# Performance work log

Hardware: AMD Instinct MI355X
Metric: run time of the kernel (lower is better)

## Reference

```python
import jax, jax.numpy as jnp
import numpy as np

N_NODES = 50000
N_EDGES = 800000
IN_DIM = 64
OUT_DIM = 128
K = 2
FINAL_DIM = IN_DIM * (2 ** (K + 1))  # 512


def _mean_agg(h, src, dst, inv_deg, n):
    # mean over neighbors: message h[src] summed into dst, normalized by in-degree
    s = jax.ops.segment_sum(h[src], dst, num_segments=n)
    return s * inv_deg[:, None]


def setup_inputs() -> dict:
    key = jax.random.key(0)
    k1, k2, k3 = jax.random.split(key, 3)
    feature = jax.random.normal(k1, (N_NODES, IN_DIM), dtype=jnp.float32)
    edge_index = jax.random.randint(k2, (2, N_EDGES), 0, N_NODES, dtype=jnp.int64)
    W = jax.random.normal(k3, (OUT_DIM, FINAL_DIM), dtype=jnp.float32) * 0.02
    b = jnp.zeros((OUT_DIM,), dtype=jnp.float32)
    return {"feature": feature, "edge_index": edge_index, "W": W, "b": b}


def reference(feature, edge_index, W, b):
    n = feature.shape[0]
    src, dst = edge_index[0], edge_index[1]
    ones = jnp.ones((src.shape[0],), dtype=feature.dtype)
    # degree normalizers (clamped to 1) for mean aggregation, each direction
    deg_in = jax.ops.segment_sum(ones, dst, num_segments=n)
    deg_out = jax.ops.segment_sum(ones, src, num_segments=n)
    inv_in = 1.0 / jnp.maximum(deg_in, 1.0)
    inv_out = 1.0 / jnp.maximum(deg_out, 1.0)

    h = feature
    for _ in range(K + 1):  # K+1 directed hops; dim doubles each hop
        h_in = _mean_agg(h, src, dst, inv_in, n)   # aggregate from in-neighbors
        h_out = _mean_agg(h, dst, src, inv_out, n)  # aggregate from out-neighbors
        h = jnp.concatenate([h_in, h_out], axis=-1)

    # output linear projection: [N, FINAL_DIM] @ [FINAL_DIM, OUT_DIM]
    return h @ W.T + b
```

## Files before the change

### kernel.cpp

```cpp
#include <hip/hip_runtime.h>

#define NN 50000
#define NE 800000
#define NBUCK 100
#define BUCK_N 500
#define CAP 10016
#define PA_BLOCKS 500
#define PA_CHUNK 1600

typedef __attribute__((ext_vector_type(8))) short short8;
typedef __attribute__((ext_vector_type(4))) float floatx4;

__device__ __forceinline__ unsigned short f2b(float x) {
    unsigned u = __float_as_uint(x);
    return (unsigned short)((u + 0x7fffu + ((u >> 16) & 1u)) >> 16);
}
__device__ __forceinline__ unsigned pk2(float lo, float hi) {
    return (unsigned)f2b(lo) | ((unsigned)f2b(hi) << 16);
}
__device__ __forceinline__ float blo(unsigned u) { return __uint_as_float(u << 16); }
__device__ __forceinline__ float bhi(unsigned u) { return __uint_as_float(u & 0xffff0000u); }
__device__ __forceinline__ void acc8(uint4 u, float* a) {
    a[0] += blo(u.x); a[1] += bhi(u.x);
    a[2] += blo(u.y); a[3] += bhi(u.y);
    a[4] += blo(u.z); a[5] += bhi(u.z);
    a[6] += blo(u.w); a[7] += bhi(u.w);
}

__global__ void featb_kernel(const float4* __restrict__ f32, uint2* __restrict__ fb) {
    int idx = blockIdx.x * 256 + threadIdx.x;
    float4 v = f32[idx];
    fb[idx] = make_uint2(pk2(v.x, v.y), pk2(v.z, v.w));
}

__global__ __launch_bounds__(256) void bucket_kernel(const int* __restrict__ src,
                                                     const int* __restrict__ dst,
                                                     int* __restrict__ gcnt_in,
                                                     int* __restrict__ gcnt_out,
                                                     int2* __restrict__ pin,
                                                     int2* __restrict__ pout) {
    __shared__ int cin[NBUCK], cout[NBUCK], rin[NBUCK], rout[NBUCK];
    int tid = threadIdx.x;
    if (tid < NBUCK) { cin[tid] = 0; cout[tid] = 0; }
    __syncthreads();
    int e0 = blockIdx.x * PA_CHUNK, e1 = e0 + PA_CHUNK;
    for (int e = e0 + tid; e < e1; e += 256) {
        atomicAdd(&cin[dst[e] / BUCK_N], 1);
        atomicAdd(&cout[src[e] / BUCK_N], 1);
    }
    __syncthreads();
    if (tid < NBUCK) {
        rin[tid]  = atomicAdd(&gcnt_in[tid], cin[tid]);
        rout[tid] = atomicAdd(&gcnt_out[tid], cout[tid]);
        cin[tid] = 0; cout[tid] = 0;
    }
    __syncthreads();
    for (int e = e0 + tid; e < e1; e += 256) {
        int s = src[e], d = dst[e];
        int bi = d / BUCK_N;
        int p = atomicAdd(&cin[bi], 1);
        pin[(size_t)bi * CAP + rin[bi] + p] = make_int2(d, s);
        int bo = s / BUCK_N;
        int q = atomicAdd(&cout[bo], 1);
        pout[(size_t)bo * CAP + rout[bo] + q] = make_int2(s, d);
    }
}

__global__ void bucket_scan_kernel(const int* __restrict__ gcnt_in,
                                   const int* __restrict__ gcnt_out,
                                   int* __restrict__ bb_in, int* __restrict__ bb_out) {
    if (threadIdx.x == 0) {
        int run = 0;
        for (int b = 0; b < NBUCK; ++b) { bb_in[b] = run; run += gcnt_in[b]; }
    }
    if (threadIdx.x == 1) {
        int run = 0;
        for (int b = 0; b < NBUCK; ++b) { bb_out[b] = run; run += gcnt_out[b]; }
    }
}

__global__ __launch_bounds__(1024) void csr_build_kernel(const int2* __restrict__ pin,
                                                         const int2* __restrict__ pout,
                                                         const int* __restrict__ gcnt_in,
                                                         const int* __restrict__ gcnt_out,
                                                         const int* __restrict__ bb_in,
                                                         const int* __restrict__ bb_out,
                                                         int* __restrict__ row_in,
                                                         int* __restrict__ row_out,
                                                         int* __restrict__ csr_in,
                                                         int* __restrict__ csr_out) {
    bool dirout = blockIdx.x >= NBUCK;
    int b = dirout ? blockIdx.x - NBUCK : blockIdx.x;
    const int2* pairs = (dirout ? pout : pin) + (size_t)b * CAP;
    int cnt  = dirout ? gcnt_out[b] : gcnt_in[b];
    int base = dirout ? bb_out[b] : bb_in[b];
    int* row = dirout ? row_out : row_in;
    int* csr = dirout ? csr_out : csr_in;
    int lo = b * BUCK_N;
    __shared__ int deg[BUCK_N], incl[BUCK_N], cur[BUCK_N];
    int tid = threadIdx.x;
    if (tid < BUCK_N) { deg[tid] = 0; cur[tid] = 0; }
    __syncthreads();
    for (int i = tid; i < cnt; i += 1024) atomicAdd(&deg[pairs[i].x - lo], 1);
    __syncthreads();
    if (tid < BUCK_N) incl[tid] = deg[tid];
    __syncthreads();
    for (int off = 1; off < BUCK_N; off <<= 1) {
        int v = 0;
        if (tid < BUCK_N && tid >= off) v = incl[tid - off];
        __syncthreads();
        if (tid < BUCK_N) incl[tid] += v;
        __syncthreads();
    }
    if (tid < BUCK_N) row[lo + tid] = base + incl[tid] - deg[tid];
    if (tid == 0 && b == NBUCK - 1) row[NN] = base + incl[BUCK_N - 1];
    __syncthreads();
    for (int i = tid; i < cnt; i += 1024) {
        int2 pr = pairs[i];
        int li = pr.x - lo;
        int pos = atomicAdd(&cur[li], 1);
        csr[base + incl[li] - deg[li] + pos] = pr.y;
    }
}

__global__ void gather1_kernel(const uint4* __restrict__ feat,
                               const int* __restrict__ row_in, const int* __restrict__ csr_in,
                               const int* __restrict__ row_out, const int* __restrict__ csr_out,
                               uint4* __restrict__ h1) {
    unsigned idx = blockIdx.x * 256 + threadIdx.x;
    unsigned n = idx >> 4, r = idx & 15;
    bool is_out = (r >= 8);
    unsigned f = r & 7;
    const int* row = is_out ? row_out : row_in;
    const int* csr = is_out ? csr_out : csr_in;
    int beg = row[n], end = row[n + 1];
    float inv = 1.0f / fmaxf((float)(end - beg), 1.0f);
    float a[8] = {};
    int j = beg;
    for (; j + 7 < end; j += 8) {
        uint4 u0 = feat[(size_t)csr[j] * 8 + f];
        uint4 u1 = feat[(size_t)csr[j + 1] * 8 + f];
        uint4 u2 = feat[(size_t)csr[j + 2] * 8 + f];
        uint4 u3 = feat[(size_t)csr[j + 3] * 8 + f];
        uint4 u4 = feat[(size_t)csr[j + 4] * 8 + f];
        uint4 u5 = feat[(size_t)csr[j + 5] * 8 + f];
        uint4 u6 = feat[(size_t)csr[j + 6] * 8 + f];
        uint4 u7 = feat[(size_t)csr[j + 7] * 8 + f];
        acc8(u0, a); acc8(u1, a); acc8(u2, a); acc8(u3, a);
        acc8(u4, a); acc8(u5, a); acc8(u6, a); acc8(u7, a);
    }
    for (; j < end; ++j) acc8(feat[(size_t)csr[j] * 8 + f], a);
    uint4 o;
    o.x = pk2(a[0] * inv, a[1] * inv);
    o.y = pk2(a[2] * inv, a[3] * inv);
    o.z = pk2(a[4] * inv, a[5] * inv);
    o.w = pk2(a[6] * inv, a[7] * inv);
    h1[(size_t)n * 16 + r] = o;
}

__global__ void gather2_kernel(const uint4* __restrict__ h1,
                               const int* __restrict__ row_in, const int* __restrict__ csr_in,
                               const int* __restrict__ row_out, const int* __restrict__ csr_out,
                               uint4* __restrict__ h2) {
    unsigned idx = blockIdx.x * 256 + threadIdx.x;
    unsigned n = idx >> 5, r = idx & 31;
    bool is_out = (r >= 16);
    unsigned f = r & 15;
    const int* row = is_out ? row_out : row_in;
    const int* csr = is_out ? csr_out : csr_in;
    int beg = row[n], end = row[n + 1];
    float inv = 1.0f / fmaxf((float)(end - beg), 1.0f);
    float a[8] = {};
    int j = beg;
    for (; j + 7 < end; j += 8) {
        uint4 u0 = h1[(size_t)csr[j] * 16 + f];
        uint4 u1 = h1[(size_t)csr[j + 1] * 16 + f];
        uint4 u2 = h1[(size_t)csr[j + 2] * 16 + f];
        uint4 u3 = h1[(size_t)csr[j + 3] * 16 + f];
        uint4 u4 = h1[(size_t)csr[j + 4] * 16 + f];
        uint4 u5 = h1[(size_t)csr[j + 5] * 16 + f];
        uint4 u6 = h1[(size_t)csr[j + 6] * 16 + f];
        uint4 u7 = h1[(size_t)csr[j + 7] * 16 + f];
        acc8(u0, a); acc8(u1, a); acc8(u2, a); acc8(u3, a);
        acc8(u4, a); acc8(u5, a); acc8(u6, a); acc8(u7, a);
    }
    for (; j < end; ++j) acc8(h1[(size_t)csr[j] * 16 + f], a);
    uint4 o;
    o.x = pk2(a[0] * inv, a[1] * inv);
    o.y = pk2(a[2] * inv, a[3] * inv);
    o.z = pk2(a[4] * inv, a[5] * inv);
    o.w = pk2(a[6] * inv, a[7] * inv);
    h2[(size_t)n * 32 + r] = o;
}

__global__ void prep_b_kernel(const float* __restrict__ W, unsigned short* __restrict__ Bnk) {
    int idx = blockIdx.x * 256 + threadIdx.x;
    int n = idx >> 8, k = idx & 255;
    float v = (n < 128) ? W[n * 512 + k] : W[(n - 128) * 512 + 256 + k];
    Bnk[idx] = f2b(v);
}

__global__ __launch_bounds__(256) void gemm_mfma_kernel(const unsigned short* __restrict__ A,
                                                        const unsigned short* __restrict__ Bnk,
                                                        unsigned short* __restrict__ C) {
    __shared__ unsigned short Bs[16][264];
    __shared__ unsigned short Cb[4][16][264];
    int tid = threadIdx.x;
    int wave = tid >> 6, lane = tid & 63;
    int l15 = lane & 15, q = lane >> 4;
    int m0 = blockIdx.x * 64;
    int mrow = m0 + wave * 16 + l15;
    int mclamp = min(mrow, NN - 1);
    const unsigned short* Arow = A + (size_t)mclamp * 256;
    short8 af[8];
#pragma unroll
    for (int s = 0; s < 8; ++s)
        af[s] = *(const short8*)(Arow + s * 32 + q * 8);
    floatx4 acc[16];
#pragma unroll
    for (int c = 0; c < 16; ++c) acc[c] = (floatx4){0.f, 0.f, 0.f, 0.f};
#pragma unroll
    for (int c = 0; c < 16; ++c) {
        {
            int nl = tid >> 4, seg = tid & 15;
            const uint4* srcp = (const uint4*)(Bnk + ((size_t)(16 * c + nl)) * 256 + seg * 16);
            uint4 v0 = srcp[0], v1 = srcp[1];
            *(uint4*)&Bs[nl][seg * 16] = v0;
            *(uint4*)&Bs[nl][seg * 16 + 8] = v1;
        }
        __syncthreads();
#pragma unroll
        for (int s = 0; s < 8; ++s) {
            short8 bf = *(const short8*)&Bs[l15][s * 32 + q * 8];
            acc[c] = __builtin_amdgcn_mfma_f32_16x16x32_bf16(af[s], bf, acc[c], 0, 0, 0);
        }
        __syncthreads();
    }
#pragma unroll
    for (int c = 0; c < 16; ++c)
#pragma unroll
        for (int r = 0; r < 4; ++r)
            Cb[wave][q * 4 + r][16 * c + l15] = f2b(acc[c][r]);
    __syncthreads();
#pragma unroll
    for (int i = 0; i < 8; ++i) {
        int t = i * 64 + lane;
        int rrow = t >> 5;
        int seg = t & 31;
        int m = m0 + wave * 16 + rrow;
        if (m < NN) {
            uint4 v = *(const uint4*)&Cb[wave][rrow][seg * 8];
            *(uint4*)(C + (size_t)m * 256 + seg * 8) = v;
        }
    }
}

__global__ void final_kernel(const uint4* __restrict__ g,
                             const int* __restrict__ row_in, const int* __restrict__ csr_in,
                             const int* __restrict__ row_out, const int* __restrict__ csr_out,
                             const float4* __restrict__ b4, float4* __restrict__ out) {
    unsigned idx = blockIdx.x * 256 + threadIdx.x;
    unsigned n = idx >> 4, f = idx & 15;
    float a[8] = {};
    {
        int beg = row_in[n], end = row_in[n + 1];
        float inv = 1.0f / fmaxf((float)(end - beg), 1.0f);
        float s[8] = {};
        int j = beg;
        for (; j + 7 < end; j += 8) {
            uint4 u0 = g[(size_t)csr_in[j] * 32 + f];
            uint4 u1 = g[(size_t)csr_in[j + 1] * 32 + f];
            uint4 u2 = g[(size_t)csr_in[j + 2] * 32 + f];
            uint4 u3 = g[(size_t)csr_in[j + 3] * 32 + f];
            uint4 u4 = g[(size_t)csr_in[j + 4] * 32 + f];
            uint4 u5 = g[(size_t)csr_in[j + 5] * 32 + f];
            uint4 u6 = g[(size_t)csr_in[j + 6] * 32 + f];
            uint4 u7 = g[(size_t)csr_in[j + 7] * 32 + f];
            acc8(u0, s); acc8(u1, s); acc8(u2, s); acc8(u3, s);
            acc8(u4, s); acc8(u5, s); acc8(u6, s); acc8(u7, s);
        }
        for (; j < end; ++j) acc8(g[(size_t)csr_in[j] * 32 + f], s);
#pragma unroll
        for (int i = 0; i < 8; ++i) a[i] += s[i] * inv;
    }
    {
        int beg = row_out[n], end = row_out[n + 1];
        float inv = 1.0f / fmaxf((float)(end - beg), 1.0f);
        float s[8] = {};
        int j = beg;
        for (; j + 7 < end; j += 8) {
            uint4 u0 = g[(size_t)csr_out[j] * 32 + 16 + f];
            uint4 u1 = g[(size_t)csr_out[j + 1] * 32 + 16 + f];
            uint4 u2 = g[(size_t)csr_out[j + 2] * 32 + 16 + f];
            uint4 u3 = g[(size_t)csr_out[j + 3] * 32 + 16 + f];
            uint4 u4 = g[(size_t)csr_out[j + 4] * 32 + 16 + f];
            uint4 u5 = g[(size_t)csr_out[j + 5] * 32 + 16 + f];
            uint4 u6 = g[(size_t)csr_out[j + 6] * 32 + 16 + f];
            uint4 u7 = g[(size_t)csr_out[j + 7] * 32 + 16 + f];
            acc8(u0, s); acc8(u1, s); acc8(u2, s); acc8(u3, s);
            acc8(u4, s); acc8(u5, s); acc8(u6, s); acc8(u7, s);
        }
        for (; j < end; ++j) acc8(g[(size_t)csr_out[j] * 32 + 16 + f], s);
#pragma unroll
        for (int i = 0; i < 8; ++i) a[i] += s[i] * inv;
    }
    float4 b0 = b4[2 * f], b1 = b4[2 * f + 1];
    out[(size_t)n * 32 + 2 * f]     = make_float4(a[0] + b0.x, a[1] + b0.y, a[2] + b0.z, a[3] + b0.w);
    out[(size_t)n * 32 + 2 * f + 1] = make_float4(a[4] + b1.x, a[5] + b1.y, a[6] + b1.z, a[7] + b1.w);
}

extern "C" void kernel_launch(void* const* d_in, const int* in_sizes, int n_in,
                              void* d_out, int out_size, void* d_ws, size_t ws_size,
                              hipStream_t stream) {
    const float* feature = (const float*)d_in[0];
    const int*   edges   = (const int*)d_in[1];
    const float* W       = (const float*)d_in[2];
    const float* b       = (const float*)d_in[3];
    const int* src = edges;
    const int* dst = edges + NE;
    float* out = (float*)d_out;

    unsigned short* featb = (unsigned short*)d_ws;
    unsigned short* h1b = featb + (size_t)NN * 64;
    unsigned short* h2b = h1b + (size_t)NN * 128;
    unsigned short* gb  = h2b + (size_t)NN * 256;
    unsigned short* Bnk = gb + (size_t)NN * 256;
    int2* pin  = (int2*)(Bnk + 65536);
    int2* pout = pin + (size_t)NBUCK * CAP;
    int* csr_in  = (int*)(pout + (size_t)NBUCK * CAP);
    int* csr_out = csr_in + NE;
    int* row_in  = csr_out + NE;
    int* row_out = row_in + NN + 1;
    int* gcnt_in  = row_out + NN + 1;
    int* gcnt_out = gcnt_in + 128;
    int* bb_in   = gcnt_out + 128;
    int* bb_out  = bb_in + 128;

    (void)hipMemsetAsync(gcnt_in, 0, 256 * sizeof(int), stream);
    featb_kernel<<<(NN * 16) / 256, 256, 0, stream>>>((const float4*)feature, (uint2*)featb);
    prep_b_kernel<<<256, 256, 0, stream>>>(W, Bnk);
    bucket_kernel<<<PA_BLOCKS, 256, 0, stream>>>(src, dst, gcnt_in, gcnt_out, pin, pout);
    bucket_scan_kernel<<<1, 64, 0, stream>>>(gcnt_in, gcnt_out, bb_in, bb_out);
    csr_build_kernel<<<2 * NBUCK, 1024, 0, stream>>>(pin, pout, gcnt_in, gcnt_out,
                                                     bb_in, bb_out, row_in, row_out,
                                                     csr_in, csr_out);

    gather1_kernel<<<(NN * 16) / 256, 256, 0, stream>>>(
        (const uint4*)featb, row_in, csr_in, row_out, csr_out, (uint4*)h1b);
    gather2_kernel<<<(NN * 32) / 256, 256, 0, stream>>>(
        (const uint4*)h1b, row_in, csr_in, row_out, csr_out, (uint4*)h2b);
    gemm_mfma_kernel<<<(NN + 63) / 64, 256, 0, stream>>>(h2b, Bnk, gb);
    final_kernel<<<(NN * 16) / 256, 256, 0, stream>>>(
        (const uint4*)gb, row_in, csr_in, row_out, csr_out, (const float4*)b, (float4*)out);
}
```

Measured before the change: 309.0 us.

## Merge prep kernels, halve gather unroll, double GEMM rows per block

Fuses the feature bf16 conversion and the weight-prep kernels into one launch that splits work by block index, removing one launch. Reduces the gather inner-loop unroll from 8 to 4 in the gather1, gather2 and final kernels, which lowers register pressure but leaves fewer loads in flight. The MFMA GEMM now handles 128 rows per block with two A tiles per wave, so each staged B tile is reused twice. That halves B reloads from global memory and barrier rounds per row, at the cost of more accumulator registers.

```diff
diff --git a/kernel.cpp b/kernel.cpp
--- a/kernel.cpp
+++ b/kernel.cpp
@@ -27,10 +27,19 @@
     a[6] += blo(u.w); a[7] += bhi(u.w);
 }
 
-__global__ void featb_kernel(const float4* __restrict__ f32, uint2* __restrict__ fb) {
-    int idx = blockIdx.x * 256 + threadIdx.x;
-    float4 v = f32[idx];
-    fb[idx] = make_uint2(pk2(v.x, v.y), pk2(v.z, v.w));
+__global__ void prep_kernel(const float4* __restrict__ f32, uint2* __restrict__ fb,
+                            const float* __restrict__ W, unsigned short* __restrict__ Bnk) {
+    int bid = blockIdx.x;
+    if (bid < 3125) {
+        int idx = bid * 256 + threadIdx.x;
+        float4 v = f32[idx];
+        fb[idx] = make_uint2(pk2(v.x, v.y), pk2(v.z, v.w));
+    } else {
+        int idx = (bid - 3125) * 256 + threadIdx.x;
+        int n = idx >> 8, k = idx & 255;
+        float v = (n < 128) ? W[n * 512 + k] : W[(n - 128) * 512 + 256 + k];
+        Bnk[idx] = f2b(v);
+    }
 }
 
 __global__ __launch_bounds__(256) void bucket_kernel(const int* __restrict__ src,
@@ -137,17 +146,12 @@
     float inv = 1.0f / fmaxf((float)(end - beg), 1.0f);
     float a[8] = {};
     int j = beg;
-    for (; j + 7 < end; j += 8) {
+    for (; j + 3 < end; j += 4) {
         uint4 u0 = feat[(size_t)csr[j] * 8 + f];
         uint4 u1 = feat[(size_t)csr[j + 1] * 8 + f];
         uint4 u2 = feat[(size_t)csr[j + 2] * 8 + f];
         uint4 u3 = feat[(size_t)csr[j + 3] * 8 + f];
-        uint4 u4 = feat[(size_t)csr[j + 4] * 8 + f];
-        uint4 u5 = feat[(size_t)csr[j + 5] * 8 + f];
-        uint4 u6 = feat[(size_t)csr[j + 6] * 8 + f];
-        uint4 u7 = feat[(size_t)csr[j + 7] * 8 + f];
         acc8(u0, a); acc8(u1, a); acc8(u2, a); acc8(u3, a);
-        acc8(u4, a); acc8(u5, a); acc8(u6, a); acc8(u7, a);
     }
     for (; j < end; ++j) acc8(feat[(size_t)csr[j] * 8 + f], a);
     uint4 o;
@@ -172,17 +176,12 @@
     float inv = 1.0f / fmaxf((float)(end - beg), 1.0f);
     float a[8] = {};
     int j = beg;
-    for (; j + 7 < end; j += 8) {
+    for (; j + 3 < end; j += 4) {
         uint4 u0 = h1[(size_t)csr[j] * 16 + f];
         uint4 u1 = h1[(size_t)csr[j + 1] * 16 + f];
         uint4 u2 = h1[(size_t)csr[j + 2] * 16 + f];
         uint4 u3 = h1[(size_t)csr[j + 3] * 16 + f];
-        uint4 u4 = h1[(size_t)csr[j + 4] * 16 + f];
-        uint4 u5 = h1[(size_t)csr[j + 5] * 16 + f];
-        uint4 u6 = h1[(size_t)csr[j + 6] * 16 + f];
-        uint4 u7 = h1[(size_t)csr[j + 7] * 16 + f];
         acc8(u0, a); acc8(u1, a); acc8(u2, a); acc8(u3, a);
-        acc8(u4, a); acc8(u5, a); acc8(u6, a); acc8(u7, a);
     }
     for (; j < end; ++j) acc8(h1[(size_t)csr[j] * 16 + f], a);
     uint4 o;
@@ -191,13 +190,6 @@
     o.z = pk2(a[4] * inv, a[5] * inv);
     o.w = pk2(a[6] * inv, a[7] * inv);
     h2[(size_t)n * 32 + r] = o;
-}
-
-__global__ void prep_b_kernel(const float* __restrict__ W, unsigned short* __restrict__ Bnk) {
-    int idx = blockIdx.x * 256 + threadIdx.x;
-    int n = idx >> 8, k = idx & 255;
-    float v = (n < 128) ? W[n * 512 + k] : W[(n - 128) * 512 + 256 + k];
-    Bnk[idx] = f2b(v);
 }
 
 __global__ __launch_bounds__(256) void gemm_mfma_kernel(const unsigned short* __restrict__ A,
@@ -208,17 +200,21 @@
     int tid = threadIdx.x;
     int wave = tid >> 6, lane = tid & 63;
     int l15 = lane & 15, q = lane >> 4;
-    int m0 = blockIdx.x * 64;
-    int mrow = m0 + wave * 16 + l15;
-    int mclamp = min(mrow, NN - 1);
-    const unsigned short* Arow = A + (size_t)mclamp * 256;
-    short8 af[8];
-#pragma unroll
-    for (int s = 0; s < 8; ++s)
-        af[s] = *(const short8*)(Arow + s * 32 + q * 8);
-    floatx4 acc[16];
-#pragma unroll
-    for (int c = 0; c < 16; ++c) acc[c] = (floatx4){0.f, 0.f, 0.f, 0.f};
+    int m0 = blockIdx.x * 128;
+    short8 af[2][8];
+#pragma unroll
+    for (int t = 0; t < 2; ++t) {
+        int mrow = m0 + (wave + 4 * t) * 16 + l15;
+        const unsigned short* Arow = A + (size_t)min(mrow, NN - 1) * 256;
+#pragma unroll
+        for (int s = 0; s < 8; ++s)
+            af[t][s] = *(const short8*)(Arow + s * 32 + q * 8);
+    }
+    floatx4 acc[2][16];
+#pragma unroll
+    for (int t = 0; t < 2; ++t)
+#pragma unroll
+        for (int c = 0; c < 16; ++c) acc[t][c] = (floatx4){0.f, 0.f, 0.f, 0.f};
 #pragma unroll
     for (int c = 0; c < 16; ++c) {
         {
@@ -232,26 +228,31 @@
 #pragma unroll
         for (int s = 0; s < 8; ++s) {
             short8 bf = *(const short8*)&Bs[l15][s * 32 + q * 8];
-            acc[c] = __builtin_amdgcn_mfma_f32_16x16x32_bf16(af[s], bf, acc[c], 0, 0, 0);
-        }
-        __syncthreads();
-    }
-#pragma unroll
-    for (int c = 0; c < 16; ++c)
-#pragma unroll
-        for (int r = 0; r < 4; ++r)
-            Cb[wave][q * 4 + r][16 * c + l15] = f2b(acc[c][r]);
-    __syncthreads();
-#pragma unroll
-    for (int i = 0; i < 8; ++i) {
-        int t = i * 64 + lane;
-        int rrow = t >> 5;
-        int seg = t & 31;
-        int m = m0 + wave * 16 + rrow;
-        if (m < NN) {
-            uint4 v = *(const uint4*)&Cb[wave][rrow][seg * 8];
-            *(uint4*)(C + (size_t)m * 256 + seg * 8) = v;
-        }
+            acc[0][c] = __builtin_amdgcn_mfma_f32_16x16x32_bf16(af[0][s], bf, acc[0][c], 0, 0, 0);
+            acc[1][c] = __builtin_amdgcn_mfma_f32_16x16x32_bf16(af[1][s], bf, acc[1][c], 0, 0, 0);
+        }
+        __syncthreads();
+    }
+#pragma unroll
+    for (int t = 0; t < 2; ++t) {
+#pragma unroll
+        for (int c = 0; c < 16; ++c)
+#pragma unroll
+            for (int r = 0; r < 4; ++r)
+                Cb[wave][q * 4 + r][16 * c + l15] = f2b(acc[t][c][r]);
+        __syncthreads();
+#pragma unroll
+        for (int i = 0; i < 8; ++i) {
+            int tt = i * 64 + lane;
+            int rrow = tt >> 5;
+            int seg = tt & 31;
+            int m = m0 + (wave + 4 * t) * 16 + rrow;
+            if (m < NN) {
+                uint4 v = *(const uint4*)&Cb[wave][rrow][seg * 8];
+                *(uint4*)(C + (size_t)m * 256 + seg * 8) = v;
+            }
+        }
+        __syncthreads();
     }
 }
 
@@ -267,17 +268,12 @@
         float inv = 1.0f / fmaxf((float)(end - beg), 1.0f);
         float s[8] = {};
         int j = beg;
-        for (; j + 7 < end; j += 8) {
+        for (; j + 3 < end; j += 4) {
             uint4 u0 = g[(size_t)csr_in[j] * 32 + f];
             uint4 u1 = g[(size_t)csr_in[j + 1] * 32 + f];
             uint4 u2 = g[(size_t)csr_in[j + 2] * 32 + f];
             uint4 u3 = g[(size_t)csr_in[j + 3] * 32 + f];
-            uint4 u4 = g[(size_t)csr_in[j + 4] * 32 + f];
-            uint4 u5 = g[(size_t)csr_in[j + 5] * 32 + f];
-            uint4 u6 = g[(size_t)csr_in[j + 6] * 32 + f];
-            uint4 u7 = g[(size_t)csr_in[j + 7] * 32 + f];
             acc8(u0, s); acc8(u1, s); acc8(u2, s); acc8(u3, s);
-            acc8(u4, s); acc8(u5, s); acc8(u6, s); acc8(u7, s);
         }
         for (; j < end; ++j) acc8(g[(size_t)csr_in[j] * 32 + f], s);
 #pragma unroll
@@ -288,17 +284,12 @@
         float inv = 1.0f / fmaxf((float)(end - beg), 1.0f);
         float s[8] = {};
         int j = beg;
-        for (; j + 7 < end; j += 8) {
+        for (; j + 3 < end; j += 4) {
             uint4 u0 = g[(size_t)csr_out[j] * 32 + 16 + f];
             uint4 u1 = g[(size_t)csr_out[j + 1] * 32 + 16 + f];
             uint4 u2 = g[(size_t)csr_out[j + 2] * 32 + 16 + f];
             uint4 u3 = g[(size_t)csr_out[j + 3] * 32 + 16 + f];
-            uint4 u4 = g[(size_t)csr_out[j + 4] * 32 + 16 + f];
-            uint4 u5 = g[(size_t)csr_out[j + 5] * 32 + 16 + f];
-            uint4 u6 = g[(size_t)csr_out[j + 6] * 32 + 16 + f];
-            uint4 u7 = g[(size_t)csr_out[j + 7] * 32 + 16 + f];
             acc8(u0, s); acc8(u1, s); acc8(u2, s); acc8(u3, s);
-            acc8(u4, s); acc8(u5, s); acc8(u6, s); acc8(u7, s);
         }
         for (; j < end; ++j) acc8(g[(size_t)csr_out[j] * 32 + 16 + f], s);
 #pragma unroll
@@ -337,8 +328,7 @@
     int* bb_out  = bb_in + 128;
 
     (void)hipMemsetAsync(gcnt_in, 0, 256 * sizeof(int), stream);
-    featb_kernel<<<(NN * 16) / 256, 256, 0, stream>>>((const float4*)feature, (uint2*)featb);
-    prep_b_kernel<<<256, 256, 0, stream>>>(W, Bnk);
+    prep_kernel<<<3125 + 256, 256, 0, stream>>>((const float4*)feature, (uint2*)featb, W, Bnk);
     bucket_kernel<<<PA_BLOCKS, 256, 0, stream>>>(src, dst, gcnt_in, gcnt_out, pin, pout);
     bucket_scan_kernel<<<1, 64, 0, stream>>>(gcnt_in, gcnt_out, bb_in, bb_out);
     csr_build_kernel<<<2 * NBUCK, 1024, 0, stream>>>(pin, pout, gcnt_in, gcnt_out,
@@ -349,7 +339,7 @@
         (const uint4*)featb, row_in, csr_in, row_out, csr_out, (uint4*)h1b);
     gather2_kernel<<<(NN * 32) / 256, 256, 0, stream>>>(
         (const uint4*)h1b, row_in, csr_in, row_out, csr_out, (uint4*)h2b);
-    gemm_mfma_kernel<<<(NN + 63) / 64, 256, 0, stream>>>(h2b, Bnk, gb);
+    gemm_mfma_kernel<<<(NN + 127) / 128, 256, 0, stream>>>(h2b, Bnk, gb);
     final_kernel<<<(NN * 16) / 256, 256, 0, stream>>>(
         (const uint4*)gb, row_in, csr_in, row_out, csr_out, (const float4*)b, (float4*)out);
 }
```

Result: faster. 271.4 us (-12.2%).
